# Optimization experiments

Hardware: AMD Instinct MI355X
Metric: run time of the kernel (lower is better)

The kernel has to match this reference:

```python
import jax, jax.numpy as jnp
from jax import lax
import numpy as np

DN = ('NHWC', 'HWIO', 'NHWC')
BN_EPS = 1e-3  # keras BatchNormalization default epsilon
# 91 threshold candidates, identical to np.arange(0, 0.91, 0.01) in otsu()
THRESH = jnp.asarray(np.arange(0.0, 0.91, 0.01), dtype=jnp.float32)


def _conv(x, w, b, s):
    return lax.conv_general_dilated(x, w, (s, s), 'SAME', dimension_numbers=DN) + b


def _convT(x, w, b, s):
    return lax.conv_transpose(x, w, (s, s), 'SAME', dimension_numbers=DN) + b


def _bn(x, p):
    g, be, m, v = p  # gamma, beta, moving_mean, moving_var (inference mode)
    return (x - m) * lax.rsqrt(v + BN_EPS) * g + be


def _otsu(error):
    # Vectorized equivalent of the nested-python-loop otsu(): for each batch
    # element, find eps in THRESH maximizing p0*p1*(mean0-mean1)^2 where
    # class0 = {err < eps}. Implemented as histogram + cumsums + argmax.
    B, n, m = error.shape
    N = n * m
    K = THRESH.shape[0]
    nb = K + 1  # bin K holds err >= THRESH[-1]
    e = error.reshape(B, N)
    # bins[b,i] = #{k : THRESH[k] <= e[b,i]}  =>  (e < THRESH[k]) <=> (bins <= k)
    bins = jnp.searchsorted(THRESH, e, side='right')
    seg = (jnp.arange(B)[:, None] * nb + bins).reshape(-1)
    counts = jax.ops.segment_sum(jnp.ones(B * N, jnp.float32), seg,
                                 num_segments=B * nb).reshape(B, nb)
    sums = jax.ops.segment_sum(e.reshape(-1), seg,
                               num_segments=B * nb).reshape(B, nb)
    c0 = jnp.cumsum(counts, axis=1)[:, :K]   # |class0| per threshold
    s0 = jnp.cumsum(sums, axis=1)[:, :K]     # sum(class0) per threshold
    tot = jnp.sum(sums, axis=1, keepdims=True)
    p0 = c0 / N
    p1 = 1.0 - p0
    mean0 = s0 / jnp.maximum(c0, 1.0)
    mean1 = (tot - s0) / jnp.maximum(N - c0, 1.0)
    sigma_w = jnp.where((c0 > 0) & (c0 < N), p0 * p1 * (mean0 - mean1) ** 2, 0.0)
    # strict-improvement loop == first argmax; all-zero sigma => threshold 0.0
    return THRESH[jnp.argmax(sigma_w, axis=1)]


def reference(x, eps_z,
              e_w1, e_b1, e_bn1, e_w2, e_b2, e_bn2, e_w3, e_b3, e_bn3,
              e_wm, e_bm, e_wv, e_bv,
              d_wd, d_bd, d_w1, d_b1, d_bn1, d_w2, d_b2, d_bn2,
              d_w3, d_b3, d_bn3, d_w4, d_b4):
    # ---- encoder (Dropout is identity at inference) ----
    h = _bn(jax.nn.relu(_conv(x, e_w1, e_b1, 2)), e_bn1)   # [B,16,16,32]
    h = _bn(jax.nn.relu(_conv(h, e_w2, e_b2, 2)), e_bn2)   # [B,8,8,64]
    h = _bn(jax.nn.relu(_conv(h, e_w3, e_b3, 2)), e_bn3)   # [B,4,4,128]
    h = h.reshape(h.shape[0], -1)                           # [B,2048]
    z_mean = jax.nn.relu(h @ e_wm + e_bm)
    z_log_var = jax.nn.relu(h @ e_wv + e_bv)
    z = z_mean + jnp.exp(0.5 * z_log_var) * eps_z           # Sampling layer
    # ---- decoder ----
    d = jax.nn.relu(z @ d_wd + d_bd).reshape(-1, 8, 8, 128)
    d = _bn(jax.nn.relu(_convT(d, d_w1, d_b1, 1)), d_bn1)   # [B,8,8,128]
    d = _bn(jax.nn.relu(_convT(d, d_w2, d_b2, 2)), d_bn2)   # [B,16,16,64]
    d = _bn(jax.nn.relu(_convT(d, d_w3, d_b3, 2)), d_bn3)   # [B,32,32,32]
    recon = jax.nn.sigmoid(_convT(d, d_w4, d_b4, 1))        # [B,32,32,3]
    # ---- per-pixel error + Otsu threshold + discriminative labelling ----
    error = jnp.mean((x - recon) ** 2, axis=-1)             # [B,32,32]
    thr = _otsu(error)                                      # [B]
    mask = (error < thr[:, None, None]).astype(jnp.int32)   # [B,32,32]
    return mask


def setup_inputs() -> dict:
    key = jax.random.key(0)
    ks = jax.random.split(key, 12)
    B = 2048
    p = lambda k, s: 0.05 * jax.random.normal(k, s, jnp.float32)
    bn = lambda c: (jnp.ones(c, jnp.float32), jnp.zeros(c, jnp.float32),
                    jnp.zeros(c, jnp.float32), jnp.ones(c, jnp.float32))
    return dict(
        x=jax.random.uniform(ks[0], (B, 32, 32, 3), jnp.float32),
        eps_z=jax.random.normal(ks[1], (B, 128), jnp.float32),
        e_w1=p(ks[2], (5, 5, 3, 32)), e_b1=jnp.zeros(32, jnp.float32), e_bn1=bn(32),
        e_w2=p(ks[3], (5, 5, 32, 64)), e_b2=jnp.zeros(64, jnp.float32), e_bn2=bn(64),
        e_w3=p(ks[4], (5, 5, 64, 128)), e_b3=jnp.zeros(128, jnp.float32), e_bn3=bn(128),
        e_wm=p(ks[5], (2048, 128)), e_bm=jnp.zeros(128, jnp.float32),
        e_wv=p(ks[6], (2048, 128)), e_bv=jnp.zeros(128, jnp.float32),
        d_wd=p(ks[7], (128, 8192)), d_bd=jnp.zeros(8192, jnp.float32),
        d_w1=p(ks[8], (1, 1, 128, 128)), d_b1=jnp.zeros(128, jnp.float32), d_bn1=bn(128),
        d_w2=p(ks[9], (3, 3, 128, 64)), d_b2=jnp.zeros(64, jnp.float32), d_bn2=bn(64),
        d_w3=p(ks[10], (3, 3, 64, 32)), d_b3=jnp.zeros(32, jnp.float32), d_bn3=bn(32),
        d_w4=p(ks[11], (3, 3, 32, 3)), d_b4=jnp.zeros(3, jnp.float32),
    )
```

## Files before the change

### kernel.cpp

```cpp
#include <hip/hip_runtime.h>
#include <math.h>

#define B_TOTAL 2048


__device__ __forceinline__ float bn_fold_scale(float g, float v) {
    return g * (float)(1.0 / sqrt((double)v + 1e-3));
}

__global__ __launch_bounds__(256) void k_conv1(
    const float* __restrict__ x, const float* __restrict__ w,
    const float* __restrict__ bias,
    const float* __restrict__ g, const float* __restrict__ be,
    const float* __restrict__ mm, const float* __restrict__ vv,
    float* __restrict__ out, int b0)
{
    __shared__ __align__(16) float sIn[3072];
    __shared__ __align__(16) float sW[2400];
    __shared__ __align__(16) float sB[32], sS[32], sBi[32];
    int t = threadIdx.x;
    const float* xin = x + (size_t)(b0 + blockIdx.x) * 3072;
    for (int i = t; i < 3072; i += 256) sIn[i] = xin[i];
    for (int i = t; i < 2400; i += 256) sW[i] = w[i];
    if (t < 32) {
        float sc = bn_fold_scale(g[t], vv[t]);
        sS[t] = sc; sBi[t] = be[t] - mm[t] * sc; sB[t] = bias[t];
    }
    __syncthreads();
    int oy = t >> 4, ox = t & 15;
    float patch[75];
#pragma unroll
    for (int kh = 0; kh < 5; ++kh) {
        int iy = 2 * oy - 1 + kh;
#pragma unroll
        for (int kw = 0; kw < 5; ++kw) {
            int ix = 2 * ox - 1 + kw;
            bool v = ((unsigned)iy < 32u) && ((unsigned)ix < 32u);
            int base = (iy * 32 + ix) * 3;
#pragma unroll
            for (int c = 0; c < 3; ++c)
                patch[(kh * 5 + kw) * 3 + c] = v ? sIn[base + c] : 0.0f;
        }
    }
    float acc[32];
#pragma unroll
    for (int i = 0; i < 32; ++i) acc[i] = 0.0f;
#pragma unroll 5
    for (int i = 0; i < 75; ++i) {
        float v = patch[i];
        const float* wr = &sW[i * 32];
#pragma unroll
        for (int q = 0; q < 8; ++q) {
            float wl[4];
            *(float4*)wl = *(const float4*)&wr[q * 4];
            acc[q*4+0] = fmaf(v, wl[0], acc[q*4+0]);
            acc[q*4+1] = fmaf(v, wl[1], acc[q*4+1]);
            acc[q*4+2] = fmaf(v, wl[2], acc[q*4+2]);
            acc[q*4+3] = fmaf(v, wl[3], acc[q*4+3]);
        }
    }
    float* o = out + ((size_t)blockIdx.x * 256 + t) * 32;
#pragma unroll
    for (int q = 0; q < 8; ++q) {
        float ov[4];
#pragma unroll
        for (int j = 0; j < 4; ++j) {
            int c = q * 4 + j;
            float r = fmaxf(acc[c] + sB[c], 0.0f);
            ov[j] = fmaf(r, sS[c], sBi[c]);
        }
        *(float4*)&o[q * 4] = *(float4*)ov;
    }
}

__global__ __launch_bounds__(256) void k_c2g(
    const float* __restrict__ in, const float* __restrict__ w,
    const float* __restrict__ bias,
    const float* __restrict__ g, const float* __restrict__ be,
    const float* __restrict__ mm, const float* __restrict__ vv,
    float* __restrict__ out)
{
    __shared__ __align__(16) float sA[32 * 132];
    __shared__ __align__(16) float sW[32 * 64];
    __shared__ __align__(16) float sB[64], sS[64], sBi[64];
    int t = threadIdx.x;
    int img0 = blockIdx.x * 2;
    if (t < 64) {
        float sc = bn_fold_scale(g[t], vv[t]);
        sS[t] = sc; sBi[t] = be[t] - mm[t] * sc; sB[t] = bias[t];
    }
    const float* in0 = in + (size_t)img0 * 8192;
    int tx = t & 15, ty = t >> 4;
    float acc[8][4];
#pragma unroll
    for (int i = 0; i < 8; ++i)
#pragma unroll
        for (int j = 0; j < 4; ++j) acc[i][j] = 0.0f;

    for (int tap = 0; tap < 25; ++tap) {
        int kh = tap / 5, kw = tap - kh * 5;
        __syncthreads();
        for (int i = t; i < 4096; i += 256) {
            int ci = i & 31, m = i >> 5;
            int im = m >> 6, pix = m & 63;
            int oy = pix >> 3, ox = pix & 7;
            int iy = 2 * oy - 1 + kh, ix = 2 * ox - 1 + kw;
            float v = ((unsigned)iy < 16u && (unsigned)ix < 16u)
                          ? in0[((size_t)im * 256 + iy * 16 + ix) * 32 + ci] : 0.0f;
            sA[ci * 132 + m] = v;
        }
        for (int i = t; i < 2048; i += 256) {
            int co = i & 63, ci = i >> 6;
            sW[ci * 64 + co] = w[((size_t)tap * 32 + ci) * 64 + co];
        }
        __syncthreads();
#pragma unroll 4
        for (int ci = 0; ci < 32; ++ci) {
            float b[4];
            *(float4*)b = *(const float4*)&sW[ci * 64 + tx * 4];
            float a0[4], a1[4];
            *(float4*)a0 = *(const float4*)&sA[ci * 132 + ty * 8];
            *(float4*)a1 = *(const float4*)&sA[ci * 132 + ty * 8 + 4];
#pragma unroll
            for (int mi = 0; mi < 4; ++mi)
#pragma unroll
                for (int j = 0; j < 4; ++j) {
                    acc[mi][j]     = fmaf(a0[mi], b[j], acc[mi][j]);
                    acc[4 + mi][j] = fmaf(a1[mi], b[j], acc[4 + mi][j]);
                }
        }
    }
    int c0 = tx * 4;
    float sc[4], bi[4], bv[4];
#pragma unroll
    for (int j = 0; j < 4; ++j) { sc[j] = sS[c0 + j]; bi[j] = sBi[c0 + j]; bv[j] = sB[c0 + j]; }
#pragma unroll
    for (int mi = 0; mi < 8; ++mi) {
        int m = ty * 8 + mi;
        int im = m >> 6, pix = m & 63;
        float ov[4];
#pragma unroll
        for (int j = 0; j < 4; ++j) {
            float r = fmaxf(acc[mi][j] + bv[j], 0.0f);
            ov[j] = fmaf(r, sc[j], bi[j]);
        }
        *(float4*)&out[((size_t)(img0 + im) * 64 + pix) * 64 + c0] = *(float4*)ov;
    }
}

__global__ __launch_bounds__(256) void k_c3g(
    const float* __restrict__ in, const float* __restrict__ w,
    const float* __restrict__ bias,
    const float* __restrict__ g, const float* __restrict__ be,
    const float* __restrict__ mm, const float* __restrict__ vv,
    float* __restrict__ out)
{
    __shared__ __align__(16) float sA[64 * 68];
    __shared__ __align__(16) float sW[64 * 128];
    __shared__ __align__(16) float sB[128], sS[128], sBi[128];
    int t = threadIdx.x;
    int img0 = blockIdx.x * 4;
    if (t < 128) {
        float sc = bn_fold_scale(g[t], vv[t]);
        sS[t] = sc; sBi[t] = be[t] - mm[t] * sc; sB[t] = bias[t];
    }
    const float* in0 = in + (size_t)img0 * 4096;
    int tx = t & 15, ty = t >> 4;
    float acc[4][8];
#pragma unroll
    for (int i = 0; i < 4; ++i)
#pragma unroll
        for (int j = 0; j < 8; ++j) acc[i][j] = 0.0f;

    for (int tap = 0; tap < 25; ++tap) {
        int kh = tap / 5, kw = tap - kh * 5;
        __syncthreads();
        for (int i = t; i < 4096; i += 256) {
            int ci = i & 63, m = i >> 6;
            int im = m >> 4, pix = m & 15;
            int oy = pix >> 2, ox = pix & 3;
            int iy = 2 * oy - 1 + kh, ix = 2 * ox - 1 + kw;
            float v = ((unsigned)iy < 8u && (unsigned)ix < 8u)
                          ? in0[((size_t)im * 64 + iy * 8 + ix) * 64 + ci] : 0.0f;
            sA[ci * 68 + m] = v;
        }
        for (int i = t; i < 8192; i += 256) {
            int co = i & 127, ci = i >> 7;
            sW[ci * 128 + co] = w[((size_t)tap * 64 + ci) * 128 + co];
        }
        __syncthreads();
#pragma unroll 2
        for (int ci = 0; ci < 64; ++ci) {
            float b[8];
            *(float4*)&b[0] = *(const float4*)&sW[ci * 128 + tx * 4];
            *(float4*)&b[4] = *(const float4*)&sW[ci * 128 + 64 + tx * 4];
            float a[4];
            *(float4*)a = *(const float4*)&sA[ci * 68 + ty * 4];
#pragma unroll
            for (int mi = 0; mi < 4; ++mi)
#pragma unroll
                for (int j = 0; j < 8; ++j)
                    acc[mi][j] = fmaf(a[mi], b[j], acc[mi][j]);
        }
    }
    int cA = tx * 4, cB = 64 + tx * 4;
#pragma unroll
    for (int mi = 0; mi < 4; ++mi) {
        int m = ty * 4 + mi;
        int im = m >> 4, pix = m & 15;
        float* o = &out[((size_t)(img0 + im) * 16 + pix) * 128];
        float ov0[4], ov1[4];
#pragma unroll
        for (int j = 0; j < 4; ++j) {
            float r = fmaxf(acc[mi][j] + sB[cA + j], 0.0f);
            ov0[j] = fmaf(r, sS[cA + j], sBi[cA + j]);
        }
#pragma unroll
        for (int j = 0; j < 4; ++j) {
            float r = fmaxf(acc[mi][4 + j] + sB[cB + j], 0.0f);
            ov1[j] = fmaf(r, sS[cB + j], sBi[cB + j]);
        }
        *(float4*)&o[cA] = *(float4*)ov0;
        *(float4*)&o[cB] = *(float4*)ov1;
    }
}

__global__ __launch_bounds__(256) void k_zpart(
    const float* __restrict__ A, const float* __restrict__ Wm,
    const float* __restrict__ Wv, float* __restrict__ part)
{
    __shared__ __align__(16) float sA[16 * 33];
    __shared__ __align__(16) float sW[32 * 256];
    int t = threadIdx.x;
    int img0 = blockIdx.x * 16;
    int k00 = blockIdx.y * 256;
    int li = t >> 4, cg = t & 15;
    float acc[16];
#pragma unroll
    for (int i = 0; i < 16; ++i) acc[i] = 0.0f;
    for (int k0 = 0; k0 < 256; k0 += 32) {
        for (int i = t; i < 512; i += 256) {
            int r = i >> 5, k = i & 31;
            sA[r * 33 + k] = A[(size_t)(img0 + r) * 2048 + k00 + k0 + k];
        }
        for (int i = t; i < 8192; i += 256) {
            int k = i >> 8, c = i & 255;
            float v = (c < 128) ? Wm[(size_t)(k00 + k0 + k) * 128 + c]
                                : Wv[(size_t)(k00 + k0 + k) * 128 + (c - 128)];
            sW[k * 256 + c] = v;
        }
        __syncthreads();
#pragma unroll 4
        for (int k = 0; k < 32; ++k) {
            float a = sA[li * 33 + k];
            const float* wr = &sW[k * 256];
#pragma unroll
            for (int q = 0; q < 4; ++q) {
                float wl[4];
                *(float4*)wl = *(const float4*)&wr[q * 64 + cg * 4];
                acc[q*4+0] = fmaf(a, wl[0], acc[q*4+0]);
                acc[q*4+1] = fmaf(a, wl[1], acc[q*4+1]);
                acc[q*4+2] = fmaf(a, wl[2], acc[q*4+2]);
                acc[q*4+3] = fmaf(a, wl[3], acc[q*4+3]);
            }
        }
        __syncthreads();
    }
    float* p = part + ((size_t)(img0 + li) * 8 + blockIdx.y) * 256;
#pragma unroll
    for (int q = 0; q < 4; ++q) {
        float4 v = make_float4(acc[q*4], acc[q*4+1], acc[q*4+2], acc[q*4+3]);
        *(float4*)&p[q * 64 + cg * 4] = v;
    }
}

__global__ __launch_bounds__(256) void k_zcombine(
    const float* __restrict__ part, const float* __restrict__ bm,
    const float* __restrict__ bv, const float* __restrict__ eps,
    float* __restrict__ z, int b0)
{
    int idx = blockIdx.x * 256 + threadIdx.x;
    int img = idx >> 7, c = idx & 127;
    const float* p = part + (size_t)img * 2048;
    float sm = 0.f, sv = 0.f;
#pragma unroll
    for (int s = 0; s < 8; ++s) { sm += p[s * 256 + c]; sv += p[s * 256 + 128 + c]; }
    float zm = fmaxf(sm + bm[c], 0.0f);
    float zlv = fmaxf(sv + bv[c], 0.0f);
    z[idx] = zm + expf(0.5f * zlv) * eps[(size_t)(b0 + img) * 128 + c];
}

__global__ __launch_bounds__(256) void k_gemm128(
    const float* __restrict__ A, const float* __restrict__ W,
    const float* __restrict__ bias,
    const float* __restrict__ g, const float* __restrict__ be,
    const float* __restrict__ mm, const float* __restrict__ vv,
    float* __restrict__ out, int N, int M)
{
    __shared__ __align__(16) float sAt[64 * 68];
    __shared__ __align__(16) float sB[64 * 68];
    int t = threadIdx.x;
    int tx = t & 15, ty = t >> 4;
    int row0 = blockIdx.x * 64, col0 = blockIdx.y * 64;
    float acc[16];
#pragma unroll
    for (int i = 0; i < 16; ++i) acc[i] = 0.0f;
    for (int kc = 0; kc < 128; kc += 64) {
        for (int i = t; i < 4096; i += 256) {
            int r = i >> 6, k = i & 63;
            sAt[k * 68 + r] = (row0 + r < M) ? A[(size_t)(row0 + r) * 128 + kc + k] : 0.0f;
        }
        for (int i = t; i < 4096; i += 256) {
            int k = i >> 6, c = i & 63;
            sB[k * 68 + c] = W[(size_t)(kc + k) * N + col0 + c];
        }
        __syncthreads();
#pragma unroll 8
        for (int k = 0; k < 64; ++k) {
            float a[4], b[4];
            *(float4*)a = *(const float4*)&sAt[k * 68 + ty * 4];
            *(float4*)b = *(const float4*)&sB[k * 68 + tx * 4];
#pragma unroll
            for (int i = 0; i < 4; ++i)
#pragma unroll
                for (int j = 0; j < 4; ++j)
                    acc[i * 4 + j] = fmaf(a[i], b[j], acc[i * 4 + j]);
        }
        __syncthreads();
    }
    int c0 = col0 + tx * 4;
    float bvv[4];
    *(float4*)bvv = *(const float4*)&bias[c0];
    float sc[4], bi[4];
    bool has_bn = (g != nullptr);
    if (has_bn) {
#pragma unroll
        for (int j = 0; j < 4; ++j) {
            float s = bn_fold_scale(g[c0 + j], vv[c0 + j]);
            sc[j] = s; bi[j] = be[c0 + j] - mm[c0 + j] * s;
        }
    }
#pragma unroll
    for (int i = 0; i < 4; ++i) {
        int row = row0 + ty * 4 + i;
        if (row >= M) continue;
        float ov[4];
#pragma unroll
        for (int j = 0; j < 4; ++j) {
            float r = fmaxf(acc[i * 4 + j] + bvv[j], 0.0f);
            ov[j] = has_bn ? fmaf(r, sc[j], bi[j]) : r;
        }
        *(float4*)&out[(size_t)row * N + c0] = *(float4*)ov;
    }
}

template <int RY, int RX>
__device__ __forceinline__ void ct2g_body(
    const float* __restrict__ xin, const float* __restrict__ w,
    float* __restrict__ sA, float* __restrict__ sW,
    const float* __restrict__ sB, const float* __restrict__ sS,
    const float* __restrict__ sBi, float* __restrict__ out_img)
{
    constexpr int NTY = RY ? 1 : 2;
    constexpr int NTX = RX ? 1 : 2;
    constexpr int T = NTY * NTX;
    constexpr int CT = (T >= 2) ? 2 : 1;
    constexpr int NCHUNK = T / CT;
    int t = threadIdx.x;
    int tx = t & 15, ty = t >> 4;
    int py = tx >> 1, px0 = (tx & 1) * 4;
    int co0 = ty * 4;
    float acc[16];
#pragma unroll
    for (int i = 0; i < 16; ++i) acc[i] = 0.0f;

    for (int pass = 0; pass < 4; ++pass) {
        int ci0 = pass * 32;
        __syncthreads();
        for (int i = t; i < 32 * 81; i += 256) {
            int ci = i & 31, pix = i >> 5;
            int r = pix / 9, c = pix - r * 9;
            int iy = r - 1, ix = c - 1;
            float v = (iy >= 0 && ix >= 0) ? xin[(iy * 8 + ix) * 128 + ci0 + ci] : 0.0f;
            sA[ci * 81 + pix] = v;
        }
#pragma unroll
        for (int chunk = 0; chunk < NCHUNK; ++chunk) {
            if (chunk) __syncthreads();
            for (int i = t; i < CT * 32 * 64; i += 256) {
                int kk = i >> 6, co = i & 63;
                int tl = kk >> 5, ci = kk & 31;
                int tt = chunk * CT + tl;
                int kh = RY ? 1 : 2 * (tt / NTX);
                int kw = RX ? 1 : 2 * (tt % NTX);
                sW[kk * 64 + co] = w[((size_t)(kh * 3 + kw) * 128 + ci0 + ci) * 64 + co];
            }
            __syncthreads();
#pragma unroll
            for (int tl = 0; tl < CT; ++tl) {
                int tt = chunk * CT + tl;
                int tY = tt / NTX, tX = tt % NTX;
                int r = RY ? (py + 1) : (py + tY);
                int cb = RX ? (px0 + 1) : (px0 + tX);
                int aB = r * 9 + cb;
                const float* wB = &sW[tl * 32 * 64 + co0];
#pragma unroll 4
                for (int ci = 0; ci < 32; ++ci) {
                    float a[4];
                    a[0] = sA[ci * 81 + aB + 0];
                    a[1] = sA[ci * 81 + aB + 1];
                    a[2] = sA[ci * 81 + aB + 2];
                    a[3] = sA[ci * 81 + aB + 3];
                    float b[4];
                    *(float4*)b = *(const float4*)&wB[ci * 64];
#pragma unroll
                    for (int i = 0; i < 4; ++i)
#pragma unroll
                        for (int j = 0; j < 4; ++j)
                            acc[i * 4 + j] = fmaf(a[i], b[j], acc[i * 4 + j]);
                }
            }
        }
    }
#pragma unroll
    for (int i = 0; i < 4; ++i) {
        int oy = 2 * py + RY, ox = 2 * (px0 + i) + RX;
        float* o = out_img + (oy * 16 + ox) * 64 + co0;
        float ov[4];
#pragma unroll
        for (int j = 0; j < 4; ++j) {
            int c = co0 + j;
            float r = fmaxf(acc[i * 4 + j] + sB[c], 0.0f);
            ov[j] = fmaf(r, sS[c], sBi[c]);
        }
        *(float4*)o = *(float4*)ov;
    }
}

__global__ __launch_bounds__(256) void k_ct2g(
    const float* __restrict__ in, const float* __restrict__ w,
    const float* __restrict__ bias,
    const float* __restrict__ g, const float* __restrict__ be,
    const float* __restrict__ mm, const float* __restrict__ vv,
    float* __restrict__ out)
{
    __shared__ __align__(16) float sA[32 * 81];
    __shared__ __align__(16) float sW[2 * 32 * 64];
    __shared__ __align__(16) float sB[64], sS[64], sBi[64];
    int t = threadIdx.x;
    if (t < 64) {
        float sc = bn_fold_scale(g[t], vv[t]);
        sS[t] = sc; sBi[t] = be[t] - mm[t] * sc; sB[t] = bias[t];
    }
    const float* xin = in + (size_t)blockIdx.x * 8192;
    float* out_img = out + (size_t)blockIdx.x * 16384;
    switch (blockIdx.y) {
        case 0:  ct2g_body<0,0>(xin, w, sA, sW, sB, sS, sBi, out_img); break;
        case 1:  ct2g_body<0,1>(xin, w, sA, sW, sB, sS, sBi, out_img); break;
        case 2:  ct2g_body<1,0>(xin, w, sA, sW, sB, sS, sBi, out_img); break;
        default: ct2g_body<1,1>(xin, w, sA, sW, sB, sS, sBi, out_img); break;
    }
}

template <int RY, int RX>
__device__ __forceinline__ void ct3g_body(
    const float* __restrict__ xin, const float* __restrict__ w,
    float* __restrict__ sA, float* __restrict__ sW,
    const float* __restrict__ sB, const float* __restrict__ sS,
    const float* __restrict__ sBi, float* __restrict__ out_img)
{
    constexpr int NTY = RY ? 1 : 2;
    constexpr int NTX = RX ? 1 : 2;
    constexpr int T = NTY * NTX;
    constexpr int CT = (T >= 2) ? 2 : 1;
    constexpr int NCHUNK = T / CT;
    int t = threadIdx.x;
    int tx = t & 63, ty = t >> 6;
    int py = tx >> 2, px0 = (tx & 3) * 4;
    int co0 = ty * 8;
    float acc[32];
#pragma unroll
    for (int i = 0; i < 32; ++i) acc[i] = 0.0f;

    for (int pass = 0; pass < 4; ++pass) {
        int ci0 = pass * 16;
        __syncthreads();
        for (int i = t; i < 16 * 289; i += 256) {
            int ci = i & 15, pix = i >> 4;
            int r = pix / 17, c = pix - r * 17;
            int iy = r - 1, ix = c - 1;
            float v = (iy >= 0 && ix >= 0) ? xin[(iy * 16 + ix) * 64 + ci0 + ci] : 0.0f;
            sA[ci * 289 + pix] = v;
        }
#pragma unroll
        for (int chunk = 0; chunk < NCHUNK; ++chunk) {
            if (chunk) __syncthreads();
            for (int i = t; i < CT * 16 * 32; i += 256) {
                int kk = i >> 5, co = i & 31;
                int tl = kk >> 4, ci = kk & 15;
                int tt = chunk * CT + tl;
                int kh = RY ? 1 : 2 * (tt / NTX);
                int kw = RX ? 1 : 2 * (tt % NTX);
                sW[kk * 32 + co] = w[((size_t)(kh * 3 + kw) * 64 + ci0 + ci) * 32 + co];
            }
            __syncthreads();
#pragma unroll
            for (int tl = 0; tl < CT; ++tl) {
                int tt = chunk * CT + tl;
                int tY = tt / NTX, tX = tt % NTX;
                int r = RY ? (py + 1) : (py + tY);
                int cb = RX ? (px0 + 1) : (px0 + tX);
                int aB = r * 17 + cb;
#pragma unroll 4
                for (int ci = 0; ci < 16; ++ci) {
                    float a[4];
                    a[0] = sA[ci * 289 + aB + 0];
                    a[1] = sA[ci * 289 + aB + 1];
                    a[2] = sA[ci * 289 + aB + 2];
                    a[3] = sA[ci * 289 + aB + 3];
                    float b[8];
                    *(float4*)&b[0] = *(const float4*)&sW[(tl * 16 + ci) * 32 + co0];
                    *(float4*)&b[4] = *(const float4*)&sW[(tl * 16 + ci) * 32 + co0 + 4];
#pragma unroll
                    for (int i = 0; i < 4; ++i)
#pragma unroll
                        for (int j = 0; j < 8; ++j)
                            acc[i * 8 + j] = fmaf(a[i], b[j], acc[i * 8 + j]);
                }
            }
        }
    }
#pragma unroll
    for (int i = 0; i < 4; ++i) {
        int oy = 2 * py + RY, ox = 2 * (px0 + i) + RX;
        float* o = out_img + (oy * 32 + ox) * 32 + co0;
        float ov0[4], ov1[4];
#pragma unroll
        for (int j = 0; j < 4; ++j) {
            int c = co0 + j;
            float r = fmaxf(acc[i * 8 + j] + sB[c], 0.0f);
            ov0[j] = fmaf(r, sS[c], sBi[c]);
        }
#pragma unroll
        for (int j = 0; j < 4; ++j) {
            int c = co0 + 4 + j;
            float r = fmaxf(acc[i * 8 + 4 + j] + sB[c], 0.0f);
            ov1[j] = fmaf(r, sS[c], sBi[c]);
        }
        *(float4*)o = *(float4*)ov0;
        *(float4*)(o + 4) = *(float4*)ov1;
    }
}

__global__ __launch_bounds__(256) void k_ct3g(
    const float* __restrict__ in, const float* __restrict__ w,
    const float* __restrict__ bias,
    const float* __restrict__ g, const float* __restrict__ be,
    const float* __restrict__ mm, const float* __restrict__ vv,
    float* __restrict__ out)
{
    __shared__ __align__(16) float sA[16 * 289];
    __shared__ __align__(16) float sW[2 * 16 * 32];
    __shared__ __align__(16) float sB[32], sS[32], sBi[32];
    int t = threadIdx.x;
    if (t < 32) {
        float sc = bn_fold_scale(g[t], vv[t]);
        sS[t] = sc; sBi[t] = be[t] - mm[t] * sc; sB[t] = bias[t];
    }
    const float* xin = in + (size_t)blockIdx.x * 16384;
    float* out_img = out + (size_t)blockIdx.x * 32768;
    switch (blockIdx.y) {
        case 0:  ct3g_body<0,0>(xin, w, sA, sW, sB, sS, sBi, out_img); break;
        case 1:  ct3g_body<0,1>(xin, w, sA, sW, sB, sS, sBi, out_img); break;
        case 2:  ct3g_body<1,0>(xin, w, sA, sW, sB, sS, sBi, out_img); break;
        default: ct3g_body<1,1>(xin, w, sA, sW, sB, sS, sBi, out_img); break;
    }
}

__global__ __launch_bounds__(256) void k_convT4_err(
    const float* __restrict__ in, const float* __restrict__ w,
    const float* __restrict__ b, const float* __restrict__ x,
    float* __restrict__ err, int b0)
{
    __shared__ __align__(16) float sIn[32 * 342];
    int t = threadIdx.x;
    int quart = blockIdx.x, img = blockIdx.y;
    int r0 = quart * 8;
    const float* xin = in + (size_t)img * 32768;
    for (int i = t; i < 10880; i += 256) {
        int pix = i >> 5, ci = i & 31;
        int lr = pix / 34;
        int cx = pix - lr * 34 - 1;
        int gy = r0 - 1 + lr;
        float v = (((unsigned)gy < 32u) && ((unsigned)cx < 32u))
                      ? xin[(gy * 32 + cx) * 32 + ci] : 0.0f;
        sIn[ci * 342 + pix] = v;
    }
    __syncthreads();
    int ly = t >> 5, lx = t & 31;
    float a0 = 0.f, a1 = 0.f, a2 = 0.f;
#pragma unroll
    for (int kh = 0; kh < 3; ++kh)
#pragma unroll
        for (int kw = 0; kw < 3; ++kw) {
            int pix = (ly + kh) * 34 + (lx + kw);
            const float* wp = w + ((kh * 3 + kw) * 32) * 3;
#pragma unroll 4
            for (int ci = 0; ci < 32; ++ci) {
                float v = sIn[ci * 342 + pix];
                a0 = fmaf(v, wp[ci * 3 + 0], a0);
                a1 = fmaf(v, wp[ci * 3 + 1], a1);
                a2 = fmaf(v, wp[ci * 3 + 2], a2);
            }
        }
    float s0 = 1.0f / (1.0f + expf(-(a0 + b[0])));
    float s1 = 1.0f / (1.0f + expf(-(a1 + b[1])));
    float s2 = 1.0f / (1.0f + expf(-(a2 + b[2])));
    int oy = r0 + ly;
    size_t xi = (((size_t)(b0 + img) * 32 + oy) * 32 + lx) * 3;
    float d0 = x[xi + 0] - s0;
    float d1 = x[xi + 1] - s1;
    float d2 = x[xi + 2] - s2;
    err[(size_t)img * 1024 + oy * 32 + lx] = (d0 * d0 + d1 * d1 + d2 * d2) * (1.0f / 3.0f);
}

__global__ __launch_bounds__(256) void k_otsu(
    const float* __restrict__ err, int* __restrict__ mask)
{
    __shared__ float sE[1024];
    __shared__ float sRed[4];
    __shared__ float sSig[96];
    __shared__ float sThr;
    int img = blockIdx.x, t = threadIdx.x;
    const float* e = err + (size_t)img * 1024;
    float part = 0.f;
    for (int i = t; i < 1024; i += 256) { float v = e[i]; sE[i] = v; part += v; }
    for (int o = 32; o; o >>= 1) part += __shfl_down(part, o);
    if ((t & 63) == 0) sRed[t >> 6] = part;
    __syncthreads();
    float tot = sRed[0] + sRed[1] + sRed[2] + sRed[3];
    if (t < 91) {
        float T = (float)((double)t * 0.01);
        int c = 0; float s = 0.f;
        for (int i = 0; i < 1024; ++i) {
            float v = sE[i];
            bool lt = v < T;
            c += lt ? 1 : 0;
            s += lt ? v : 0.0f;
        }
        float cf = (float)c;
        float p0 = cf * (1.0f / 1024.0f);
        float p1 = 1.0f - p0;
        float m0 = s / fmaxf(cf, 1.0f);
        float m1 = (tot - s) / fmaxf(1024.0f - cf, 1.0f);
        float d = m0 - m1;
        sSig[t] = (c > 0 && c < 1024) ? (p0 * p1) * (d * d) : 0.0f;
    }
    __syncthreads();
    if (t == 0) {
        float best = sSig[0]; int bk = 0;
        for (int k = 1; k < 91; ++k)
            if (sSig[k] > best) { best = sSig[k]; bk = k; }
        sThr = (float)((double)bk * 0.01);
    }
    __syncthreads();
    float thr = sThr;
    int* m = mask + (size_t)img * 1024;
    for (int i = t; i < 1024; i += 256) m[i] = (sE[i] < thr) ? 1 : 0;
}

extern "C" void kernel_launch(void* const* d_in, const int* in_sizes, int n_in,
                              void* d_out, int out_size, void* d_ws, size_t ws_size,
                              hipStream_t stream)
{
    (void)in_sizes; (void)out_size;
    const float* p[46];
    bool flat = (n_in >= 46);
    if (flat) {
        for (int i = 0; i < 46; ++i) p[i] = (const float*)d_in[i];
    } else {
        int o = 0;
        int s = 0;
        auto leaf = [&](int count) {
            for (int j = 0; j < count; ++j) p[o++] = (const float*)d_in[s++];
        };
        auto bn4 = [&](int C) {
            const float* base = (const float*)d_in[s++];
            p[o++] = base; p[o++] = base + C; p[o++] = base + 2 * C; p[o++] = base + 3 * C;
        };
        leaf(2);
        leaf(2); bn4(32);
        leaf(2); bn4(64);
        leaf(2); bn4(128);
        leaf(4);
        leaf(2);
        leaf(2); bn4(128);
        leaf(2); bn4(64);
        leaf(2); bn4(32);
        leaf(2);
    }
    const float* x      = p[0];
    const float* epsz   = p[1];
    const float* e_w1   = p[2];
    const float* e_b1   = p[3];
    const float* e_bn1g = p[4], *e_bn1b = p[5], *e_bn1m = p[6], *e_bn1v = p[7];
    const float* e_w2   = p[8];
    const float* e_b2   = p[9];
    const float* e_bn2g = p[10], *e_bn2b = p[11], *e_bn2m = p[12], *e_bn2v = p[13];
    const float* e_w3   = p[14];
    const float* e_b3   = p[15];
    const float* e_bn3g = p[16], *e_bn3b = p[17], *e_bn3m = p[18], *e_bn3v = p[19];
    const float* e_wm   = p[20];
    const float* e_bm   = p[21];
    const float* e_wv   = p[22];
    const float* e_bv   = p[23];
    const float* d_wd   = p[24];
    const float* d_bd   = p[25];
    const float* d_w1   = p[26];
    const float* d_b1   = p[27];
    const float* d_bn1g = p[28], *d_bn1b = p[29], *d_bn1m = p[30], *d_bn1v = p[31];
    const float* d_w2   = p[32];
    const float* d_b2   = p[33];
    const float* d_bn2g = p[34], *d_bn2b = p[35], *d_bn2m = p[36], *d_bn2v = p[37];
    const float* d_w3   = p[38];
    const float* d_b3   = p[39];
    const float* d_bn3g = p[40], *d_bn3b = p[41], *d_bn3m = p[42], *d_bn3v = p[43];
    const float* d_w4   = p[44];
    const float* d_b4   = p[45];
    int* mask = (int*)d_out;

    float* ws = (float*)d_ws;
    int Bc = B_TOTAL;
    while (Bc > 16) {
        size_t need = (size_t)Bc * 50304u * 4u;
        if (need <= ws_size) break;
        Bc >>= 1;
    }
    float* err = ws;
    float* z   = err + (size_t)Bc * 1024;
    float* P   = z + (size_t)Bc * 128;
    float* Q   = P + (size_t)Bc * 16384;

    for (int b0 = 0; b0 < B_TOTAL; b0 += Bc) {
        k_conv1<<<Bc, 256, 0, stream>>>(x, e_w1, e_b1, e_bn1g, e_bn1b, e_bn1m, e_bn1v, P, b0);
        k_c2g<<<Bc / 2, 256, 0, stream>>>(P, e_w2, e_b2, e_bn2g, e_bn2b, e_bn2m, e_bn2v, Q);
        k_c3g<<<Bc / 4, 256, 0, stream>>>(Q, e_w3, e_b3, e_bn3g, e_bn3b, e_bn3m, e_bn3v, P);
        k_zpart<<<dim3(Bc / 16, 8), 256, 0, stream>>>(P, e_wm, e_wv, Q);
        k_zcombine<<<(Bc * 128) / 256, 256, 0, stream>>>(Q, e_bm, e_bv, epsz, z, b0);
        k_gemm128<<<dim3((Bc + 63) / 64, 128), 256, 0, stream>>>(z, d_wd, d_bd,
            nullptr, nullptr, nullptr, nullptr, P, 8192, Bc);
        k_gemm128<<<dim3(Bc, 2), 256, 0, stream>>>(P, d_w1, d_b1,
            d_bn1g, d_bn1b, d_bn1m, d_bn1v, Q, 128, Bc * 64);
        k_ct2g<<<dim3(Bc, 4), 256, 0, stream>>>(Q, d_w2, d_b2, d_bn2g, d_bn2b, d_bn2m, d_bn2v, P);
        k_ct3g<<<dim3(Bc, 4), 256, 0, stream>>>(P, d_w3, d_b3, d_bn3g, d_bn3b, d_bn3m, d_bn3v, Q);
        k_convT4_err<<<dim3(4, Bc), 256, 0, stream>>>(Q, d_w4, d_b4, x, err, b0);
        k_otsu<<<Bc, 256, 0, stream>>>(err, mask + (size_t)b0 * 1024);
    }
}
```

Baseline: 2.297 ms.

## Batch multiple images per block in transposed-conv kernels to reuse weights

```diff
diff --git a/kernel.cpp b/kernel.cpp
--- a/kernel.cpp
+++ b/kernel.cpp
@@ -356,224 +356,254 @@
 
 template <int RY, int RX>
 __device__ __forceinline__ void ct2g_body(
-    const float* __restrict__ xin, const float* __restrict__ w,
+    const float* __restrict__ in0, const float* __restrict__ w,
     float* __restrict__ sA, float* __restrict__ sW,
     const float* __restrict__ sB, const float* __restrict__ sS,
-    const float* __restrict__ sBi, float* __restrict__ out_img)
+    const float* __restrict__ sBi, float* __restrict__ out0)
 {
     constexpr int NTY = RY ? 1 : 2;
     constexpr int NTX = RX ? 1 : 2;
-    constexpr int T = NTY * NTX;
-    constexpr int CT = (T >= 2) ? 2 : 1;
-    constexpr int NCHUNK = T / CT;
-    int t = threadIdx.x;
-    int tx = t & 15, ty = t >> 4;
-    int py = tx >> 1, px0 = (tx & 1) * 4;
-    int co0 = ty * 4;
-    float acc[16];
-#pragma unroll
-    for (int i = 0; i < 16; ++i) acc[i] = 0.0f;
-
-    for (int pass = 0; pass < 4; ++pass) {
-        int ci0 = pass * 32;
-        __syncthreads();
-        for (int i = t; i < 32 * 81; i += 256) {
-            int ci = i & 31, pix = i >> 5;
-            int r = pix / 9, c = pix - r * 9;
-            int iy = r - 1, ix = c - 1;
-            float v = (iy >= 0 && ix >= 0) ? xin[(iy * 8 + ix) * 128 + ci0 + ci] : 0.0f;
-            sA[ci * 81 + pix] = v;
-        }
-#pragma unroll
-        for (int chunk = 0; chunk < NCHUNK; ++chunk) {
-            if (chunk) __syncthreads();
-            for (int i = t; i < CT * 32 * 64; i += 256) {
+    constexpr int TT = NTY * NTX;
+    int t = threadIdx.x;
+    int px0 = (t & 1) * 4;
+    int py  = (t >> 1) & 7;
+    int u   = (t >> 4) & 1;
+    int ty  = t >> 5;
+    int co0 = ty * 8;
+    int imgA = 2 * u, imgB = 2 * u + 1;
+    float acc0[4][8], acc1[4][8];
+#pragma unroll
+    for (int i = 0; i < 4; ++i)
+#pragma unroll
+        for (int j = 0; j < 8; ++j) { acc0[i][j] = 0.0f; acc1[i][j] = 0.0f; }
+
+    for (int pass = 0; pass < 8; ++pass) {
+        int ci0 = pass * 16;
+        __syncthreads();
+        for (int img = 0; img < 4; ++img) {
+            const float* xin = in0 + (size_t)img * 8192;
+            for (int i = t; i < 16 * 81; i += 256) {
+                int ci = i & 15, pix = i >> 4;
+                int r = pix / 9, c = pix - r * 9;
+                int iy = r - 1, ix = c - 1;
+                float v = (iy >= 0 && ix >= 0) ? xin[(iy * 8 + ix) * 128 + ci0 + ci] : 0.0f;
+                sA[(img * 16 + ci) * 81 + pix] = v;
+            }
+        }
+        for (int tb = 0; tb < TT; tb += 2) {
+            if (tb) __syncthreads();
+            for (int i = t; i < 2 * 16 * 64; i += 256) {
                 int kk = i >> 6, co = i & 63;
-                int tl = kk >> 5, ci = kk & 31;
-                int tt = chunk * CT + tl;
+                int tl = kk >> 4, ci = kk & 15;
+                int tt = tb + tl; if (tt >= TT) tt = TT - 1;
                 int kh = RY ? 1 : 2 * (tt / NTX);
                 int kw = RX ? 1 : 2 * (tt % NTX);
                 sW[kk * 64 + co] = w[((size_t)(kh * 3 + kw) * 128 + ci0 + ci) * 64 + co];
             }
             __syncthreads();
 #pragma unroll
-            for (int tl = 0; tl < CT; ++tl) {
-                int tt = chunk * CT + tl;
+            for (int tl = 0; tl < 2; ++tl) {
+                int tt = tb + tl;
+                if (tt >= TT) break;
                 int tY = tt / NTX, tX = tt % NTX;
                 int r = RY ? (py + 1) : (py + tY);
                 int cb = RX ? (px0 + 1) : (px0 + tX);
                 int aB = r * 9 + cb;
-                const float* wB = &sW[tl * 32 * 64 + co0];
 #pragma unroll 4
-                for (int ci = 0; ci < 32; ++ci) {
-                    float a[4];
-                    a[0] = sA[ci * 81 + aB + 0];
-                    a[1] = sA[ci * 81 + aB + 1];
-                    a[2] = sA[ci * 81 + aB + 2];
-                    a[3] = sA[ci * 81 + aB + 3];
-                    float b[4];
-                    *(float4*)b = *(const float4*)&wB[ci * 64];
+                for (int ci = 0; ci < 16; ++ci) {
+                    float b[8];
+                    *(float4*)&b[0] = *(const float4*)&sW[(tl * 16 + ci) * 64 + co0];
+                    *(float4*)&b[4] = *(const float4*)&sW[(tl * 16 + ci) * 64 + co0 + 4];
+                    float a0[4], a1[4];
+                    const float* pA = &sA[(imgA * 16 + ci) * 81 + aB];
+                    const float* pB = &sA[(imgB * 16 + ci) * 81 + aB];
+                    a0[0] = pA[0]; a0[1] = pA[1]; a0[2] = pA[2]; a0[3] = pA[3];
+                    a1[0] = pB[0]; a1[1] = pB[1]; a1[2] = pB[2]; a1[3] = pB[3];
 #pragma unroll
                     for (int i = 0; i < 4; ++i)
 #pragma unroll
-                        for (int j = 0; j < 4; ++j)
-                            acc[i * 4 + j] = fmaf(a[i], b[j], acc[i * 4 + j]);
+                        for (int j = 0; j < 8; ++j) {
+                            acc0[i][j] = fmaf(a0[i], b[j], acc0[i][j]);
+                            acc1[i][j] = fmaf(a1[i], b[j], acc1[i][j]);
+                        }
                 }
             }
         }
     }
 #pragma unroll
-    for (int i = 0; i < 4; ++i) {
-        int oy = 2 * py + RY, ox = 2 * (px0 + i) + RX;
-        float* o = out_img + (oy * 16 + ox) * 64 + co0;
-        float ov[4];
-#pragma unroll
-        for (int j = 0; j < 4; ++j) {
-            int c = co0 + j;
-            float r = fmaxf(acc[i * 4 + j] + sB[c], 0.0f);
-            ov[j] = fmaf(r, sS[c], sBi[c]);
-        }
-        *(float4*)o = *(float4*)ov;
-    }
-}
-
-__global__ __launch_bounds__(256) void k_ct2g(
+    for (int l = 0; l < 2; ++l) {
+        int img = 2 * u + l;
+        float* oimg = out0 + (size_t)img * 16384;
+#pragma unroll
+        for (int i = 0; i < 4; ++i) {
+            int oy = 2 * py + RY, ox = 2 * (px0 + i) + RX;
+            float* o = oimg + (oy * 16 + ox) * 64 + co0;
+            float ov0[4], ov1[4];
+#pragma unroll
+            for (int j = 0; j < 4; ++j) {
+                int c = co0 + j;
+                float r = fmaxf((l ? acc1[i][j] : acc0[i][j]) + sB[c], 0.0f);
+                ov0[j] = fmaf(r, sS[c], sBi[c]);
+            }
+#pragma unroll
+            for (int j = 0; j < 4; ++j) {
+                int c = co0 + 4 + j;
+                float r = fmaxf((l ? acc1[i][4 + j] : acc0[i][4 + j]) + sB[c], 0.0f);
+                ov1[j] = fmaf(r, sS[c], sBi[c]);
+            }
+            *(float4*)o = *(float4*)ov0;
+            *(float4*)(o + 4) = *(float4*)ov1;
+        }
+    }
+}
+
+__global__ __launch_bounds__(256, 4) void k_ct2g(
     const float* __restrict__ in, const float* __restrict__ w,
     const float* __restrict__ bias,
     const float* __restrict__ g, const float* __restrict__ be,
     const float* __restrict__ mm, const float* __restrict__ vv,
     float* __restrict__ out)
 {
-    __shared__ __align__(16) float sA[32 * 81];
-    __shared__ __align__(16) float sW[2 * 32 * 64];
+    __shared__ __align__(16) float sA[4 * 16 * 81];
+    __shared__ __align__(16) float sW[2 * 16 * 64];
     __shared__ __align__(16) float sB[64], sS[64], sBi[64];
     int t = threadIdx.x;
     if (t < 64) {
         float sc = bn_fold_scale(g[t], vv[t]);
         sS[t] = sc; sBi[t] = be[t] - mm[t] * sc; sB[t] = bias[t];
     }
-    const float* xin = in + (size_t)blockIdx.x * 8192;
-    float* out_img = out + (size_t)blockIdx.x * 16384;
+    const float* in0 = in + (size_t)blockIdx.x * 4 * 8192;
+    float* out0 = out + (size_t)blockIdx.x * 4 * 16384;
     switch (blockIdx.y) {
-        case 0:  ct2g_body<0,0>(xin, w, sA, sW, sB, sS, sBi, out_img); break;
-        case 1:  ct2g_body<0,1>(xin, w, sA, sW, sB, sS, sBi, out_img); break;
-        case 2:  ct2g_body<1,0>(xin, w, sA, sW, sB, sS, sBi, out_img); break;
-        default: ct2g_body<1,1>(xin, w, sA, sW, sB, sS, sBi, out_img); break;
+        case 0:  ct2g_body<0,0>(in0, w, sA, sW, sB, sS, sBi, out0); break;
+        case 1:  ct2g_body<0,1>(in0, w, sA, sW, sB, sS, sBi, out0); break;
+        case 2:  ct2g_body<1,0>(in0, w, sA, sW, sB, sS, sBi, out0); break;
+        default: ct2g_body<1,1>(in0, w, sA, sW, sB, sS, sBi, out0); break;
     }
 }
 
 template <int RY, int RX>
 __device__ __forceinline__ void ct3g_body(
-    const float* __restrict__ xin, const float* __restrict__ w,
+    const float* __restrict__ in0, const float* __restrict__ w,
     float* __restrict__ sA, float* __restrict__ sW,
     const float* __restrict__ sB, const float* __restrict__ sS,
-    const float* __restrict__ sBi, float* __restrict__ out_img)
+    const float* __restrict__ sBi, float* __restrict__ out0)
 {
     constexpr int NTY = RY ? 1 : 2;
     constexpr int NTX = RX ? 1 : 2;
-    constexpr int T = NTY * NTX;
-    constexpr int CT = (T >= 2) ? 2 : 1;
-    constexpr int NCHUNK = T / CT;
-    int t = threadIdx.x;
-    int tx = t & 63, ty = t >> 6;
-    int py = tx >> 2, px0 = (tx & 3) * 4;
+    constexpr int TT = NTY * NTX;
+    int t = threadIdx.x;
+    int px0 = (t & 3) * 4;
+    int py  = (t >> 2) & 15;
+    int ty  = t >> 6;
     int co0 = ty * 8;
-    float acc[32];
-#pragma unroll
-    for (int i = 0; i < 32; ++i) acc[i] = 0.0f;
-
-    for (int pass = 0; pass < 4; ++pass) {
-        int ci0 = pass * 16;
-        __syncthreads();
-        for (int i = t; i < 16 * 289; i += 256) {
-            int ci = i & 15, pix = i >> 4;
-            int r = pix / 17, c = pix - r * 17;
-            int iy = r - 1, ix = c - 1;
-            float v = (iy >= 0 && ix >= 0) ? xin[(iy * 16 + ix) * 64 + ci0 + ci] : 0.0f;
-            sA[ci * 289 + pix] = v;
-        }
-#pragma unroll
-        for (int chunk = 0; chunk < NCHUNK; ++chunk) {
-            if (chunk) __syncthreads();
-            for (int i = t; i < CT * 16 * 32; i += 256) {
+    float acc0[4][8], acc1[4][8];
+#pragma unroll
+    for (int i = 0; i < 4; ++i)
+#pragma unroll
+        for (int j = 0; j < 8; ++j) { acc0[i][j] = 0.0f; acc1[i][j] = 0.0f; }
+
+    for (int pass = 0; pass < 8; ++pass) {
+        int ci0 = pass * 8;
+        __syncthreads();
+        for (int img = 0; img < 2; ++img) {
+            const float* xin = in0 + (size_t)img * 16384;
+            for (int i = t; i < 8 * 289; i += 256) {
+                int ci = i & 7, pix = i >> 3;
+                int r = pix / 17, c = pix - r * 17;
+                int iy = r - 1, ix = c - 1;
+                float v = (iy >= 0 && ix >= 0) ? xin[(iy * 16 + ix) * 64 + ci0 + ci] : 0.0f;
+                sA[(img * 8 + ci) * 289 + pix] = v;
+            }
+        }
+        for (int tb = 0; tb < TT; tb += 2) {
+            if (tb) __syncthreads();
+            for (int i = t; i < 2 * 8 * 32; i += 256) {
                 int kk = i >> 5, co = i & 31;
-                int tl = kk >> 4, ci = kk & 15;
-                int tt = chunk * CT + tl;
+                int tl = kk >> 3, ci = kk & 7;
+                int tt = tb + tl; if (tt >= TT) tt = TT - 1;
                 int kh = RY ? 1 : 2 * (tt / NTX);
                 int kw = RX ? 1 : 2 * (tt % NTX);
                 sW[kk * 32 + co] = w[((size_t)(kh * 3 + kw) * 64 + ci0 + ci) * 32 + co];
             }
             __syncthreads();
 #pragma unroll
-            for (int tl = 0; tl < CT; ++tl) {
-                int tt = chunk * CT + tl;
+            for (int tl = 0; tl < 2; ++tl) {
+                int tt = tb + tl;
+                if (tt >= TT) break;
                 int tY = tt / NTX, tX = tt % NTX;
                 int r = RY ? (py + 1) : (py + tY);
                 int cb = RX ? (px0 + 1) : (px0 + tX);
                 int aB = r * 17 + cb;
 #pragma unroll 4
-                for (int ci = 0; ci < 16; ++ci) {
-                    float a[4];
-                    a[0] = sA[ci * 289 + aB + 0];
-                    a[1] = sA[ci * 289 + aB + 1];
-                    a[2] = sA[ci * 289 + aB + 2];
-                    a[3] = sA[ci * 289 + aB + 3];
+                for (int ci = 0; ci < 8; ++ci) {
                     float b[8];
-                    *(float4*)&b[0] = *(const float4*)&sW[(tl * 16 + ci) * 32 + co0];
-                    *(float4*)&b[4] = *(const float4*)&sW[(tl * 16 + ci) * 32 + co0 + 4];
+                    *(float4*)&b[0] = *(const float4*)&sW[(tl * 8 + ci) * 32 + co0];
+                    *(float4*)&b[4] = *(const float4*)&sW[(tl * 8 + ci) * 32 + co0 + 4];
+                    float a0[4], a1[4];
+                    const float* pA = &sA[ci * 289 + aB];
+                    const float* pB = &sA[(8 + ci) * 289 + aB];
+                    a0[0] = pA[0]; a0[1] = pA[1]; a0[2] = pA[2]; a0[3] = pA[3];
+                    a1[0] = pB[0]; a1[1] = pB[1]; a1[2] = pB[2]; a1[3] = pB[3];
 #pragma unroll
                     for (int i = 0; i < 4; ++i)
 #pragma unroll
-                        for (int j = 0; j < 8; ++j)
-                            acc[i * 8 + j] = fmaf(a[i], b[j], acc[i * 8 + j]);
+                        for (int j = 0; j < 8; ++j) {
+                            acc0[i][j] = fmaf(a0[i], b[j], acc0[i][j]);
+                            acc1[i][j] = fmaf(a1[i], b[j], acc1[i][j]);
+                        }
                 }
             }
         }
     }
 #pragma unroll
-    for (int i = 0; i < 4; ++i) {
-        int oy = 2 * py + RY, ox = 2 * (px0 + i) + RX;
-        float* o = out_img + (oy * 32 + ox) * 32 + co0;
-        float ov0[4], ov1[4];
-#pragma unroll
-        for (int j = 0; j < 4; ++j) {
-            int c = co0 + j;
-            float r = fmaxf(acc[i * 8 + j] + sB[c], 0.0f);
-            ov0[j] = fmaf(r, sS[c], sBi[c]);
-        }
-#pragma unroll
-        for (int j = 0; j < 4; ++j) {
-            int c = co0 + 4 + j;
-            float r = fmaxf(acc[i * 8 + 4 + j] + sB[c], 0.0f);
-            ov1[j] = fmaf(r, sS[c], sBi[c]);
-        }
-        *(float4*)o = *(float4*)ov0;
-        *(float4*)(o + 4) = *(float4*)ov1;
-    }
-}
-
-__global__ __launch_bounds__(256) void k_ct3g(
+    for (int l = 0; l < 2; ++l) {
+        float* oimg = out0 + (size_t)l * 32768;
+#pragma unroll
+        for (int i = 0; i < 4; ++i) {
+            int oy = 2 * py + RY, ox = 2 * (px0 + i) + RX;
+            float* o = oimg + (oy * 32 + ox) * 32 + co0;
+            float ov0[4], ov1[4];
+#pragma unroll
+            for (int j = 0; j < 4; ++j) {
+                int c = co0 + j;
+                float r = fmaxf((l ? acc1[i][j] : acc0[i][j]) + sB[c], 0.0f);
+                ov0[j] = fmaf(r, sS[c], sBi[c]);
+            }
+#pragma unroll
+            for (int j = 0; j < 4; ++j) {
+                int c = co0 + 4 + j;
+                float r = fmaxf((l ? acc1[i][4 + j] : acc0[i][4 + j]) + sB[c], 0.0f);
+                ov1[j] = fmaf(r, sS[c], sBi[c]);
+            }
+            *(float4*)o = *(float4*)ov0;
+            *(float4*)(o + 4) = *(float4*)ov1;
+        }
+    }
+}
+
+__global__ __launch_bounds__(256, 4) void k_ct3g(
     const float* __restrict__ in, const float* __restrict__ w,
     const float* __restrict__ bias,
     const float* __restrict__ g, const float* __restrict__ be,
     const float* __restrict__ mm, const float* __restrict__ vv,
     float* __restrict__ out)
 {
-    __shared__ __align__(16) float sA[16 * 289];
-    __shared__ __align__(16) float sW[2 * 16 * 32];
+    __shared__ __align__(16) float sA[2 * 8 * 289];
+    __shared__ __align__(16) float sW[2 * 8 * 32];
     __shared__ __align__(16) float sB[32], sS[32], sBi[32];
     int t = threadIdx.x;
     if (t < 32) {
         float sc = bn_fold_scale(g[t], vv[t]);
         sS[t] = sc; sBi[t] = be[t] - mm[t] * sc; sB[t] = bias[t];
     }
-    const float* xin = in + (size_t)blockIdx.x * 16384;
-    float* out_img = out + (size_t)blockIdx.x * 32768;
+    const float* in0 = in + (size_t)blockIdx.x * 2 * 16384;
+    float* out0 = out + (size_t)blockIdx.x * 2 * 32768;
     switch (blockIdx.y) {
-        case 0:  ct3g_body<0,0>(xin, w, sA, sW, sB, sS, sBi, out_img); break;
-        case 1:  ct3g_body<0,1>(xin, w, sA, sW, sB, sS, sBi, out_img); break;
-        case 2:  ct3g_body<1,0>(xin, w, sA, sW, sB, sS, sBi, out_img); break;
-        default: ct3g_body<1,1>(xin, w, sA, sW, sB, sS, sBi, out_img); break;
+        case 0:  ct3g_body<0,0>(in0, w, sA, sW, sB, sS, sBi, out0); break;
+        case 1:  ct3g_body<0,1>(in0, w, sA, sW, sB, sS, sBi, out0); break;
+        case 2:  ct3g_body<1,0>(in0, w, sA, sW, sB, sS, sBi, out0); break;
+        default: ct3g_body<1,1>(in0, w, sA, sW, sB, sS, sBi, out0); break;
     }
 }
 
@@ -751,8 +781,8 @@
             nullptr, nullptr, nullptr, nullptr, P, 8192, Bc);
         k_gemm128<<<dim3(Bc, 2), 256, 0, stream>>>(P, d_w1, d_b1,
             d_bn1g, d_bn1b, d_bn1m, d_bn1v, Q, 128, Bc * 64);
-        k_ct2g<<<dim3(Bc, 4), 256, 0, stream>>>(Q, d_w2, d_b2, d_bn2g, d_bn2b, d_bn2m, d_bn2v, P);
-        k_ct3g<<<dim3(Bc, 4), 256, 0, stream>>>(P, d_w3, d_b3, d_bn3g, d_bn3b, d_bn3m, d_bn3v, Q);
+        k_ct2g<<<dim3(Bc / 4, 4), 256, 0, stream>>>(Q, d_w2, d_b2, d_bn2g, d_bn2b, d_bn2m, d_bn2v, P);
+        k_ct3g<<<dim3(Bc / 2, 4), 256, 0, stream>>>(P, d_w3, d_b3, d_bn3g, d_bn3b, d_bn3m, d_bn3v, Q);
         k_convT4_err<<<dim3(4, Bc), 256, 0, stream>>>(Q, d_w4, d_b4, x, err, b0);
         k_otsu<<<Bc, 256, 0, stream>>>(err, mask + (size_t)b0 * 1024);
     }
```

New measurement: 2.246 ms. 2.2% less time.
